# Performance work log

Measured on AMD Instinct MI355X. Metric: run time of the kernel, lower is better.

## Reference

```python
import jax, jax.numpy as jnp
import numpy as np

B, C, H, W = 8, 32, 256, 256


def setup_inputs() -> dict:
    key = jax.random.key(0)
    ks = jax.random.split(key, 9)
    x = jax.random.normal(ks[0], (B, C, H, W), dtype=jnp.float32)
    # depthwise 1x1 conv (groups=C) == per-channel scalar weight + bias
    def wb(kw, kb):
        w = jax.random.normal(kw, (C,), dtype=jnp.float32) * (1.0 / jnp.sqrt(1.0))
        b = jax.random.normal(kb, (C,), dtype=jnp.float32) * 0.1
        return w, b
    w_up, b_up = wb(ks[1], ks[2])
    w_right, b_right = wb(ks[3], ks[4])
    w_down, b_down = wb(ks[5], ks[6])
    w_left, b_left = wb(ks[7], ks[8])
    return {"x": x, "w_up": w_up, "b_up": b_up, "w_right": w_right,
            "b_right": b_right, "w_down": w_down, "b_down": b_down,
            "w_left": w_left, "b_left": b_left}


def _dir_scan(x_seq, w, b):
    """x_seq: [L, B, C, K]. h[0]=x[0]; h[t+1]=relu(w_c*h[t]+b_c+x[t+1])."""
    wb_ = w[None, :, None]
    bb_ = b[None, :, None]

    def step(h, xt):
        hn = jax.nn.relu(h * wb_ + bb_ + xt)
        return hn, hn

    _, ys = jax.lax.scan(step, x_seq[0], x_seq[1:])
    return jnp.concatenate([x_seq[:1], ys], axis=0)


def reference(x, w_up, b_up, w_right, b_right, w_down, b_down, w_left, b_left):
    xh = jnp.moveaxis(x, 2, 0)  # [H, B, C, W] for row scans
    xw = jnp.moveaxis(x, 3, 0)  # [W, B, C, H] for column scans

    top_down = jnp.moveaxis(_dir_scan(xh, w_down, b_down), 0, 2)
    top_up = jnp.moveaxis(_dir_scan(xh[::-1], w_up, b_up)[::-1], 0, 2)
    top_right = jnp.moveaxis(_dir_scan(xw, w_right, b_right), 0, 3)
    top_left = jnp.moveaxis(_dir_scan(xw[::-1], w_left, b_left)[::-1], 0, 3)

    return (top_up, top_right, top_down, top_left)
```

## Files before the change

### kernel.cpp

```cpp
#include <hip/hip_runtime.h>

#define BB 8
#define CC 32
#define HH 256
#define WW 256

typedef float vf2 __attribute__((ext_vector_type(2)));
typedef float vf4 __attribute__((ext_vector_type(4)));

__device__ __forceinline__ float step_v9(float h, float w, float bx) {
    float t = __fmaf_rn(h, w, bx);
    float r;
    asm volatile("v_med3_f32 %0, %1, 0, %2"
                 : "=v"(r)
                 : "v"(t), "v"(3.3895313892515355e+38f));
    return r;
}

#define LDS_BARRIER() asm volatile("s_waitcnt lgkmcnt(0)\n\ts_barrier" ::: "memory")

__global__ __launch_bounds__(256, 4) void irnn_fused_v9(
    const float* __restrict__ x,
    const float* __restrict__ w_up,    const float* __restrict__ b_up,
    const float* __restrict__ w_right, const float* __restrict__ b_right,
    const float* __restrict__ w_down,  const float* __restrict__ b_down,
    const float* __restrict__ w_left,  const float* __restrict__ b_left,
    float* __restrict__ out_up, float* __restrict__ out_right,
    float* __restrict__ out_down, float* __restrict__ out_left)
{
    __shared__ float tile[256 * 33];

    const int p    = blockIdx.x;
    const int x8   = p & 7;
    const int slot = p >> 3;
    const int pg   = slot / 3;
    const int role = slot - pg * 3;
    const int bc   = pg * 8 + x8;
    const int c    = bc & (CC - 1);

    if (role == 0) {
        const int down = (threadIdx.x < 128);
        const int t    = threadIdx.x & 127;
        const int w2   = t * 2;
        const float wc = down ? w_down[c] : w_up[c];
        const float bv = down ? b_down[c] : b_up[c];

        const long long base = (long long)bc * (HH * WW) + w2;
        const long long st   = down ? WW : -WW;
        const long long off0 = down ? 0 : (long long)(HH - 1) * WW;
        const float* xs = x + base + off0;
        float*       os = (down ? out_down : out_up) + base + off0;

        vf2 h = *(const vf2*)xs;
        __builtin_nontemporal_store(h, (vf2*)os);

        vf2 buf[8];
        #pragma unroll
        for (int i = 0; i < 8; ++i) buf[i] = *(const vf2*)(xs + (1 + i) * st);

        int kb = 1;
        #pragma unroll 1
        for (int g = 0; g < 30; ++g) {
            vf2 nb[8];
            #pragma unroll
            for (int i = 0; i < 8; ++i) nb[i] = *(const vf2*)(xs + (kb + 8 + i) * st);
            #pragma unroll
            for (int i = 0; i < 8; ++i) {
                h.x = step_v9(h.x, wc, __fadd_rn(bv, buf[i].x));
                h.y = step_v9(h.y, wc, __fadd_rn(bv, buf[i].y));
                __builtin_nontemporal_store(h, (vf2*)(os + (kb + i) * st));
            }
            #pragma unroll
            for (int i = 0; i < 8; ++i) buf[i] = nb[i];
            kb += 8;
        }
        vf2 tb[7];
        #pragma unroll
        for (int i = 0; i < 7; ++i) tb[i] = *(const vf2*)(xs + (249 + i) * st);
        #pragma unroll
        for (int i = 0; i < 8; ++i) {
            h.x = step_v9(h.x, wc, __fadd_rn(bv, buf[i].x));
            h.y = step_v9(h.y, wc, __fadd_rn(bv, buf[i].y));
            __builtin_nontemporal_store(h, (vf2*)(os + (241 + i) * st));
        }
        #pragma unroll
        for (int i = 0; i < 7; ++i) {
            h.x = step_v9(h.x, wc, __fadd_rn(bv, tb[i].x));
            h.y = step_v9(h.y, wc, __fadd_rn(bv, tb[i].y));
            __builtin_nontemporal_store(h, (vf2*)(os + (249 + i) * st));
        }
        return;
    }

    const int dir = role - 1;
    const int tid = threadIdx.x;
    const float wc = dir ? w_left[c] : w_right[c];
    const float bv = dir ? b_left[c] : b_right[c];
    const float* xbase = x + (long long)bc * (HH * WW);
    float* obase = (dir ? out_left : out_right) + (long long)bc * (HH * WW);

    vf4 st4[8];

    {
        const int w0 = dir ? (7 * 32) : 0;
        #pragma unroll
        for (int it = 0; it < 8; ++it) {
            int idx = it * 256 + tid;
            int row = idx >> 3, l = idx & 7;
            st4[it] = *(const vf4*)(xbase + row * WW + w0 + l * 4);
        }
        #pragma unroll
        for (int it = 0; it < 8; ++it) {
            int idx = it * 256 + tid;
            int row = idx >> 3, l = idx & 7;
            int a = row * 33 + l * 4;
            tile[a]     = st4[it].x;
            tile[a + 1] = st4[it].y;
            tile[a + 2] = st4[it].z;
            tile[a + 3] = st4[it].w;
        }
    }
    LDS_BARRIER();

    float h = 0.0f;
    float* trow = &tile[tid * 33];
    #pragma unroll 1
    for (int s = 0; s < 8; ++s) {
        const int cur = dir ? (7 - s) : s;
        const int w0c = cur * 32;

        if (s < 7) {
            const int nw0 = (dir ? (6 - s) : (s + 1)) * 32;
            #pragma unroll
            for (int it = 0; it < 8; ++it) {
                int idx = it * 256 + tid;
                int row = idx >> 3, l = idx & 7;
                st4[it] = *(const vf4*)(xbase + row * WW + nw0 + l * 4);
            }
        }

        {
            float rb[32];
            #pragma unroll
            for (int i = 0; i < 32; ++i) rb[i] = trow[i];
            if (dir == 0) {
                if (s == 0) {
                    h = rb[0]; trow[0] = h;
                    #pragma unroll
                    for (int i = 1; i < 32; ++i) {
                        h = step_v9(h, wc, __fadd_rn(bv, rb[i]));
                        trow[i] = h;
                    }
                } else {
                    #pragma unroll
                    for (int i = 0; i < 32; ++i) {
                        h = step_v9(h, wc, __fadd_rn(bv, rb[i]));
                        trow[i] = h;
                    }
                }
            } else {
                if (s == 0) {
                    h = rb[31]; trow[31] = h;
                    #pragma unroll
                    for (int i = 30; i >= 0; --i) {
                        h = step_v9(h, wc, __fadd_rn(bv, rb[i]));
                        trow[i] = h;
                    }
                } else {
                    #pragma unroll
                    for (int i = 31; i >= 0; --i) {
                        h = step_v9(h, wc, __fadd_rn(bv, rb[i]));
                        trow[i] = h;
                    }
                }
            }
        }
        LDS_BARRIER();

        #pragma unroll
        for (int it = 0; it < 8; ++it) {
            int idx = it * 256 + tid;
            int row = idx >> 3, l = idx & 7;
            int a = row * 33 + l * 4;
            vf4 v;
            v.x = tile[a];
            v.y = tile[a + 1];
            v.z = tile[a + 2];
            v.w = tile[a + 3];
            __builtin_nontemporal_store(v, (vf4*)(obase + row * WW + w0c + l * 4));
            if (s < 7) {
                tile[a]     = st4[it].x;
                tile[a + 1] = st4[it].y;
                tile[a + 2] = st4[it].z;
                tile[a + 3] = st4[it].w;
            }
        }
        LDS_BARRIER();
    }
}

extern "C" void kernel_launch(void* const* d_in, const int* in_sizes, int n_in,
                              void* d_out, int out_size, void* d_ws, size_t ws_size,
                              hipStream_t stream) {
    const float* x       = (const float*)d_in[0];
    const float* w_up    = (const float*)d_in[1];
    const float* b_up    = (const float*)d_in[2];
    const float* w_right = (const float*)d_in[3];
    const float* b_right = (const float*)d_in[4];
    const float* w_down  = (const float*)d_in[5];
    const float* b_down  = (const float*)d_in[6];
    const float* w_left  = (const float*)d_in[7];
    const float* b_left  = (const float*)d_in[8];

    float* out = (float*)d_out;
    const long long N = (long long)BB * CC * HH * WW;
    float* out_up    = out;
    float* out_right = out + N;
    float* out_down  = out + 2 * N;
    float* out_left  = out + 3 * N;

    irnn_fused_v9<<<dim3(768), 256, 0, stream>>>(
        x, w_up, b_up, w_right, b_right, w_down, b_down, w_left, b_left,
        out_up, out_right, out_down, out_left);
}
```

Before: 333.9 us.

## Rebalance work split: vertical blocks handle two planes with vf4, LDS uses vf2

Vertical (up/down) scan blocks now cover two planes each, with 64 threads per direction per plane using 4-wide vector loads and stores. Horizontal blocks stay one per plane and direction, so the grid drops from 768 to 640 blocks with 5 roles per plane pair. The LDS row stride goes from 33 to 34 so the tile can use 8-byte vf2 accesses, and the row scan loads its data in two prefetched halves. The aim is fewer memory instructions and a better balance between vertical and horizontal blocks. The costs are more registers per vertical thread and possible LDS bank conflicts with the even stride.

Measured after the change: 334.8 us. Within noise of the previous version (+0.3%).

```diff
diff --git a/kernel.cpp b/kernel.cpp
--- a/kernel.cpp
+++ b/kernel.cpp
@@ -4,11 +4,12 @@
 #define CC 32
 #define HH 256
 #define WW 256
+#define HST 34
 
 typedef float vf2 __attribute__((ext_vector_type(2)));
 typedef float vf4 __attribute__((ext_vector_type(4)));
 
-__device__ __forceinline__ float step_v9(float h, float w, float bx) {
+__device__ __forceinline__ float stepf(float h, float w, float bx) {
     float t = __fmaf_rn(h, w, bx);
     float r;
     asm volatile("v_med3_f32 %0, %1, 0, %2"
@@ -19,7 +20,7 @@
 
 #define LDS_BARRIER() asm volatile("s_waitcnt lgkmcnt(0)\n\ts_barrier" ::: "memory")
 
-__global__ __launch_bounds__(256, 4) void irnn_fused_v9(
+__global__ __launch_bounds__(256, 4) void irnn_fused_v10(
     const float* __restrict__ x,
     const float* __restrict__ w_up,    const float* __restrict__ b_up,
     const float* __restrict__ w_right, const float* __restrict__ b_right,
@@ -28,76 +29,86 @@
     float* __restrict__ out_up, float* __restrict__ out_right,
     float* __restrict__ out_down, float* __restrict__ out_left)
 {
-    __shared__ float tile[256 * 33];
+    __shared__ float tile[256 * HST];
 
     const int p    = blockIdx.x;
     const int x8   = p & 7;
     const int slot = p >> 3;
-    const int pg   = slot / 3;
-    const int role = slot - pg * 3;
-    const int bc   = pg * 8 + x8;
-    const int c    = bc & (CC - 1);
+    const int pr   = slot / 5;
+    const int role = slot - pr * 5;
+    const int pair = pr * 8 + x8;
 
     if (role == 0) {
-        const int down = (threadIdx.x < 128);
-        const int t    = threadIdx.x & 127;
-        const int w2   = t * 2;
+        const int sub   = threadIdx.x >> 6;
+        const int lane  = threadIdx.x & 63;
+        const int plane = pair * 2 + (sub >> 1);
+        const int down  = ((sub & 1) == 0);
+        const int c     = plane & (CC - 1);
+        const int col   = lane * 4;
         const float wc = down ? w_down[c] : w_up[c];
         const float bv = down ? b_down[c] : b_up[c];
 
-        const long long base = (long long)bc * (HH * WW) + w2;
+        const long long base = (long long)plane * (HH * WW) + col;
         const long long st   = down ? WW : -WW;
         const long long off0 = down ? 0 : (long long)(HH - 1) * WW;
         const float* xs = x + base + off0;
         float*       os = (down ? out_down : out_up) + base + off0;
 
-        vf2 h = *(const vf2*)xs;
-        __builtin_nontemporal_store(h, (vf2*)os);
-
-        vf2 buf[8];
-        #pragma unroll
-        for (int i = 0; i < 8; ++i) buf[i] = *(const vf2*)(xs + (1 + i) * st);
+        vf4 h = *(const vf4*)xs;
+        __builtin_nontemporal_store(h, (vf4*)os);
+
+        vf4 buf[8];
+        #pragma unroll
+        for (int i = 0; i < 8; ++i) buf[i] = *(const vf4*)(xs + (1 + i) * st);
 
         int kb = 1;
         #pragma unroll 1
         for (int g = 0; g < 30; ++g) {
-            vf2 nb[8];
-            #pragma unroll
-            for (int i = 0; i < 8; ++i) nb[i] = *(const vf2*)(xs + (kb + 8 + i) * st);
+            vf4 nb[8];
+            #pragma unroll
+            for (int i = 0; i < 8; ++i) nb[i] = *(const vf4*)(xs + (kb + 8 + i) * st);
             #pragma unroll
             for (int i = 0; i < 8; ++i) {
-                h.x = step_v9(h.x, wc, __fadd_rn(bv, buf[i].x));
-                h.y = step_v9(h.y, wc, __fadd_rn(bv, buf[i].y));
-                __builtin_nontemporal_store(h, (vf2*)(os + (kb + i) * st));
+                h.x = stepf(h.x, wc, __fadd_rn(bv, buf[i].x));
+                h.y = stepf(h.y, wc, __fadd_rn(bv, buf[i].y));
+                h.z = stepf(h.z, wc, __fadd_rn(bv, buf[i].z));
+                h.w = stepf(h.w, wc, __fadd_rn(bv, buf[i].w));
+                __builtin_nontemporal_store(h, (vf4*)(os + (kb + i) * st));
             }
             #pragma unroll
             for (int i = 0; i < 8; ++i) buf[i] = nb[i];
             kb += 8;
         }
-        vf2 tb[7];
-        #pragma unroll
-        for (int i = 0; i < 7; ++i) tb[i] = *(const vf2*)(xs + (249 + i) * st);
+        vf4 tb[7];
+        #pragma unroll
+        for (int i = 0; i < 7; ++i) tb[i] = *(const vf4*)(xs + (249 + i) * st);
         #pragma unroll
         for (int i = 0; i < 8; ++i) {
-            h.x = step_v9(h.x, wc, __fadd_rn(bv, buf[i].x));
-            h.y = step_v9(h.y, wc, __fadd_rn(bv, buf[i].y));
-            __builtin_nontemporal_store(h, (vf2*)(os + (241 + i) * st));
+            h.x = stepf(h.x, wc, __fadd_rn(bv, buf[i].x));
+            h.y = stepf(h.y, wc, __fadd_rn(bv, buf[i].y));
+            h.z = stepf(h.z, wc, __fadd_rn(bv, buf[i].z));
+            h.w = stepf(h.w, wc, __fadd_rn(bv, buf[i].w));
+            __builtin_nontemporal_store(h, (vf4*)(os + (241 + i) * st));
         }
         #pragma unroll
         for (int i = 0; i < 7; ++i) {
-            h.x = step_v9(h.x, wc, __fadd_rn(bv, tb[i].x));
-            h.y = step_v9(h.y, wc, __fadd_rn(bv, tb[i].y));
-            __builtin_nontemporal_store(h, (vf2*)(os + (249 + i) * st));
+            h.x = stepf(h.x, wc, __fadd_rn(bv, tb[i].x));
+            h.y = stepf(h.y, wc, __fadd_rn(bv, tb[i].y));
+            h.z = stepf(h.z, wc, __fadd_rn(bv, tb[i].z));
+            h.w = stepf(h.w, wc, __fadd_rn(bv, tb[i].w));
+            __builtin_nontemporal_store(h, (vf4*)(os + (249 + i) * st));
         }
         return;
     }
 
-    const int dir = role - 1;
-    const int tid = threadIdx.x;
+    const int plane = pair * 2 + ((role - 1) >> 1);
+    const int dir   = (role - 1) & 1;
+    const int c     = plane & (CC - 1);
+    const int tid   = threadIdx.x;
     const float wc = dir ? w_left[c] : w_right[c];
     const float bv = dir ? b_left[c] : b_right[c];
-    const float* xbase = x + (long long)bc * (HH * WW);
-    float* obase = (dir ? out_left : out_right) + (long long)bc * (HH * WW);
+    const float* xbase = x + (long long)plane * (HH * WW);
+    float* obase = (dir ? out_left : out_right) + (long long)plane * (HH * WW);
 
     vf4 st4[8];
 
@@ -113,17 +124,15 @@
         for (int it = 0; it < 8; ++it) {
             int idx = it * 256 + tid;
             int row = idx >> 3, l = idx & 7;
-            int a = row * 33 + l * 4;
-            tile[a]     = st4[it].x;
-            tile[a + 1] = st4[it].y;
-            tile[a + 2] = st4[it].z;
-            tile[a + 3] = st4[it].w;
+            int a = row * HST + l * 4;
+            *(vf2*)&tile[a]     = vf2{st4[it].x, st4[it].y};
+            *(vf2*)&tile[a + 2] = vf2{st4[it].z, st4[it].w};
         }
     }
     LDS_BARRIER();
 
     float h = 0.0f;
-    float* trow = &tile[tid * 33];
+    float* trow = &tile[tid * HST];
     #pragma unroll 1
     for (int s = 0; s < 8; ++s) {
         const int cur = dir ? (7 - s) : s;
@@ -139,39 +148,50 @@
             }
         }
 
-        {
-            float rb[32];
-            #pragma unroll
-            for (int i = 0; i < 32; ++i) rb[i] = trow[i];
-            if (dir == 0) {
-                if (s == 0) {
-                    h = rb[0]; trow[0] = h;
-                    #pragma unroll
-                    for (int i = 1; i < 32; ++i) {
-                        h = step_v9(h, wc, __fadd_rn(bv, rb[i]));
-                        trow[i] = h;
-                    }
-                } else {
-                    #pragma unroll
-                    for (int i = 0; i < 32; ++i) {
-                        h = step_v9(h, wc, __fadd_rn(bv, rb[i]));
-                        trow[i] = h;
-                    }
-                }
-            } else {
-                if (s == 0) {
-                    h = rb[31]; trow[31] = h;
-                    #pragma unroll
-                    for (int i = 30; i >= 0; --i) {
-                        h = step_v9(h, wc, __fadd_rn(bv, rb[i]));
-                        trow[i] = h;
-                    }
-                } else {
-                    #pragma unroll
-                    for (int i = 31; i >= 0; --i) {
-                        h = step_v9(h, wc, __fadd_rn(bv, rb[i]));
-                        trow[i] = h;
-                    }
+        if (dir == 0) {
+            vf2 rb[8], nb[8];
+            #pragma unroll
+            for (int j = 0; j < 8; ++j) rb[j] = *(const vf2*)&trow[2 * j];
+            #pragma unroll
+            for (int q = 0; q < 2; ++q) {
+                if (q == 0) {
+                    #pragma unroll
+                    for (int j = 0; j < 8; ++j) nb[j] = *(const vf2*)&trow[16 + 2 * j];
+                }
+                #pragma unroll
+                for (int j = 0; j < 8; ++j) {
+                    float lo;
+                    if (s == 0 && q == 0 && j == 0) lo = rb[0].x;
+                    else lo = stepf(h, wc, __fadd_rn(bv, rb[j].x));
+                    h = stepf(lo, wc, __fadd_rn(bv, rb[j].y));
+                    *(vf2*)&trow[q * 16 + 2 * j] = vf2{lo, h};
+                }
+                if (q == 0) {
+                    #pragma unroll
+                    for (int j = 0; j < 8; ++j) rb[j] = nb[j];
+                }
+            }
+        } else {
+            vf2 rb[8], nb[8];
+            #pragma unroll
+            for (int j = 0; j < 8; ++j) rb[j] = *(const vf2*)&trow[16 + 2 * j];
+            #pragma unroll
+            for (int q = 0; q < 2; ++q) {
+                if (q == 0) {
+                    #pragma unroll
+                    for (int j = 0; j < 8; ++j) nb[j] = *(const vf2*)&trow[2 * j];
+                }
+                #pragma unroll
+                for (int j = 7; j >= 0; --j) {
+                    float hi;
+                    if (s == 0 && q == 0 && j == 7) hi = rb[7].y;
+                    else hi = stepf(h, wc, __fadd_rn(bv, rb[j].y));
+                    h = stepf(hi, wc, __fadd_rn(bv, rb[j].x));
+                    *(vf2*)&trow[(1 - q) * 16 + 2 * j] = vf2{h, hi};
+                }
+                if (q == 0) {
+                    #pragma unroll
+                    for (int j = 0; j < 8; ++j) rb[j] = nb[j];
                 }
             }
         }
@@ -181,18 +201,14 @@
         for (int it = 0; it < 8; ++it) {
             int idx = it * 256 + tid;
             int row = idx >> 3, l = idx & 7;
-            int a = row * 33 + l * 4;
-            vf4 v;
-            v.x = tile[a];
-            v.y = tile[a + 1];
-            v.z = tile[a + 2];
-            v.w = tile[a + 3];
+            int a = row * HST + l * 4;
+            vf2 v0 = *(const vf2*)&tile[a];
+            vf2 v1 = *(const vf2*)&tile[a + 2];
+            vf4 v; v.x = v0.x; v.y = v0.y; v.z = v1.x; v.w = v1.y;
             __builtin_nontemporal_store(v, (vf4*)(obase + row * WW + w0c + l * 4));
             if (s < 7) {
-                tile[a]     = st4[it].x;
-                tile[a + 1] = st4[it].y;
-                tile[a + 2] = st4[it].z;
-                tile[a + 3] = st4[it].w;
+                *(vf2*)&tile[a]     = vf2{st4[it].x, st4[it].y};
+                *(vf2*)&tile[a + 2] = vf2{st4[it].z, st4[it].w};
             }
         }
         LDS_BARRIER();
@@ -219,7 +235,7 @@
     float* out_down  = out + 2 * N;
     float* out_left  = out + 3 * N;
 
-    irnn_fused_v9<<<dim3(768), 256, 0, stream>>>(
+    irnn_fused_v10<<<dim3(640), 256, 0, stream>>>(
         x, w_up, b_up, w_right, b_right, w_down, b_down, w_left, b_left,
         out_up, out_right, out_down, out_left);
 }
```
